# Optimization experiments

Hardware: AMD Instinct MI355X
Metric: run time of the kernel (lower is better)

The kernel has to match this reference:

```python
import jax, jax.numpy as jnp
import numpy as np

N_NODES = 100000
N_EDGES = 320000
EF_DIM = 128
HID = 128          # hidden_dim == time_dim
D_IN = EF_DIM + HID  # predictor input dim
Q = 4096


def setup_inputs() -> dict:
    key = jax.random.key(0)
    ks = jax.random.split(key, 16)
    src = jax.random.randint(ks[0], (N_EDGES,), 0, N_NODES, dtype=jnp.int32)
    dst = jax.random.randint(ks[1], (N_EDGES,), 0, N_NODES, dtype=jnp.int32)
    ef = jax.random.normal(ks[2], (N_EDGES, EF_DIM), dtype=jnp.float32)
    bt = jax.random.uniform(ks[3], (N_EDGES,), dtype=jnp.float32)
    node_ts = jax.random.uniform(ks[4], (N_NODES,), dtype=jnp.float32)
    s_idx = jax.random.randint(ks[5], (Q,), 0, N_NODES, dtype=jnp.int32)
    p_idx = jax.random.randint(ks[6], (Q,), 0, N_NODES, dtype=jnp.int32)
    n_idx = jax.random.randint(ks[7], (Q,), 0, N_NODES, dtype=jnp.int32)
    # TimeEncode weights: w = 1/10**linspace(0,9,HID), bias = 0
    time_w = jnp.asarray(1.0 / 10 ** np.linspace(0, 9, HID), dtype=jnp.float32)
    time_b = jnp.zeros((HID,), dtype=jnp.float32)
    sc1 = 1.0 / np.sqrt(D_IN)
    sc2 = 1.0 / np.sqrt(HID)
    W_src = jax.random.normal(ks[8], (D_IN, HID), dtype=jnp.float32) * sc1
    b_src = jnp.zeros((HID,), dtype=jnp.float32)
    W_dst = jax.random.normal(ks[9], (D_IN, HID), dtype=jnp.float32) * sc1
    b_dst = jnp.zeros((HID,), dtype=jnp.float32)
    W_out = jax.random.normal(ks[10], (HID, 1), dtype=jnp.float32) * sc2
    b_out = jnp.zeros((1,), dtype=jnp.float32)
    return {
        "src": src, "dst": dst, "ef": ef, "bt": bt, "node_ts": node_ts,
        "s_idx": s_idx, "p_idx": p_idx, "n_idx": n_idx,
        "time_w": time_w, "time_b": time_b,
        "W_src": W_src, "b_src": b_src,
        "W_dst": W_dst, "b_dst": b_dst,
        "W_out": W_out, "b_out": b_out,
    }


def reference(src, dst, ef, bt, node_ts, s_idx, p_idx, n_idx,
              time_w, time_b, W_src, b_src, W_dst, b_dst, W_out, b_out):
    n_nodes = node_ts.shape[0]
    # TemporalEdgePreprocess: time_diff = edge_ts - src_node_ts; cos(w*t + b)
    time_diff = bt - node_ts[src]                              # [E]
    tenc = jnp.cos(time_diff[:, None] * time_w[None, :] + time_b[None, :])  # [E, HID]
    efeat = jnp.concatenate([ef, tenc], axis=1)                # [E, D_IN]
    # update_all(copy_e, sum): segment-sum edge features into destination nodes
    h = jax.ops.segment_sum(efeat, dst, num_segments=n_nodes)  # [N, D_IN]
    s_emb = h[s_idx]                                           # [Q, D_IN]
    p_emb = h[p_idx]
    n_emb = h[n_idx]
    # EdgePredictor (neg_samples=1, so tile is identity)
    h_src = s_emb @ W_src + b_src
    h_pos = p_emb @ W_dst + b_dst
    h_neg = n_emb @ W_dst + b_dst
    pos_logit = jax.nn.relu(h_src + h_pos) @ W_out + b_out     # [Q, 1]
    neg_logit = jax.nn.relu(h_src + h_neg) @ W_out + b_out     # [Q, 1]
    return pos_logit, neg_logit
```

## Files before the change

kernel.cpp:

```cpp
#include <hip/hip_runtime.h>

#define N_NODES 100000
#define N_EDGES 320000
#define Q 4096
#define HID 128
#define DIN 256
#define EMB_LD 260
#define NSLOT (3 * Q)
#define CAP 64
#define QPB 8
#define KT 32

__global__ __launch_bounds__(256) void k_init(int4* __restrict__ slot4) {
    int i = blockIdx.x * 256 + threadIdx.x;
    if (i < N_NODES / 4) slot4[i] = make_int4(-1, -1, -1, -1);
}

__global__ __launch_bounds__(256) void k_claim(const int* __restrict__ s_idx,
                                               const int* __restrict__ p_idx,
                                               const int* __restrict__ n_idx,
                                               int* __restrict__ slot,
                                               int* __restrict__ cnt) {
    int i = blockIdx.x * 256 + threadIdx.x;
    cnt[i] = 0;
    int t = i >> 12;
    int q = i & (Q - 1);
    int node = (t == 0 ? s_idx : (t == 1 ? p_idx : n_idx))[q];
    atomicCAS(&slot[node], -1, i);
}

__global__ __launch_bounds__(256) void k_build(
    const int* __restrict__ src, const int* __restrict__ dst,
    const float* __restrict__ bt, const float* __restrict__ node_ts,
    const int* __restrict__ slot, int* __restrict__ cnt,
    int2* __restrict__ edata) {
    int e = blockIdx.x * 256 + threadIdx.x;
    if (e >= N_EDGES) return;
    int sl = slot[dst[e]];
    if (sl < 0) return;
    float td = bt[e] - node_ts[src[e]];
    int pos = atomicAdd(&cnt[sl], 1);
    if (pos < CAP) edata[sl * CAP + pos] = make_int2(e, __float_as_int(td));
}

__global__ __launch_bounds__(256) void k_fused(
    const int* __restrict__ s_idx, const int* __restrict__ p_idx,
    const int* __restrict__ n_idx, const int* __restrict__ slot,
    const int* __restrict__ cnt, const int2* __restrict__ edata,
    const float* __restrict__ ef,
    const float* __restrict__ time_w, const float* __restrict__ time_b,
    const float* __restrict__ W_src, const float* __restrict__ b_src,
    const float* __restrict__ W_dst, const float* __restrict__ b_dst,
    const float* __restrict__ W_out, const float* __restrict__ b_out,
    float* __restrict__ out) {
    __shared__ float emb[QPB * 3][EMB_LD];
    __shared__ float wstage[2][KT][HID];
    __shared__ float pP[QPB][4], pN[QPB][4];
    const int tid   = threadIdx.x;
    const int qbase = blockIdx.x * QPB;
    const int w     = tid >> 6;
    const int lane  = tid & 63;

    {
        const int j = lane >> 4;
        const int g = lane & 15;
        const float4 tw0 = *reinterpret_cast<const float4*>(time_w + 8 * g);
        const float4 tw1 = *reinterpret_cast<const float4*>(time_w + 8 * g + 4);
        const float4 tb0 = *reinterpret_cast<const float4*>(time_b + 8 * g);
        const float4 tb1 = *reinterpret_cast<const float4*>(time_b + 8 * g + 4);
        for (int row = w; row < QPB * 3; row += 4) {
            int t = row >> 3, q = row & 7;
            const int* ia = (t == 0) ? s_idx : (t == 1) ? p_idx : n_idx;
            int sl = slot[ia[qbase + q]];
            int n = cnt[sl]; if (n > CAP) n = CAP;
            float4 accA = {0.f, 0.f, 0.f, 0.f}, accB = {0.f, 0.f, 0.f, 0.f};
            float4 tcA  = {0.f, 0.f, 0.f, 0.f}, tcB  = {0.f, 0.f, 0.f, 0.f};
            for (int jb = j; jb < n; jb += 4) {
                int2 ed = edata[(size_t)sl * CAP + jb];
                const float* rp = ef + (size_t)ed.x * 128;
                float4 vA = *reinterpret_cast<const float4*>(rp + 4 * g);
                float4 vB = *reinterpret_cast<const float4*>(rp + 64 + 4 * g);
                float td = __int_as_float(ed.y);
                accA.x += vA.x; accA.y += vA.y; accA.z += vA.z; accA.w += vA.w;
                accB.x += vB.x; accB.y += vB.y; accB.z += vB.z; accB.w += vB.w;
                tcA.x += __cosf(td * tw0.x + tb0.x);
                tcA.y += __cosf(td * tw0.y + tb0.y);
                tcA.z += __cosf(td * tw0.z + tb0.z);
                tcA.w += __cosf(td * tw0.w + tb0.w);
                tcB.x += __cosf(td * tw1.x + tb1.x);
                tcB.y += __cosf(td * tw1.y + tb1.y);
                tcB.z += __cosf(td * tw1.z + tb1.z);
                tcB.w += __cosf(td * tw1.w + tb1.w);
            }
#define RED2(v) { v += __shfl_xor(v, 16); v += __shfl_xor(v, 32); }
            RED2(accA.x) RED2(accA.y) RED2(accA.z) RED2(accA.w)
            RED2(accB.x) RED2(accB.y) RED2(accB.z) RED2(accB.w)
            RED2(tcA.x)  RED2(tcA.y)  RED2(tcA.z)  RED2(tcA.w)
            RED2(tcB.x)  RED2(tcB.y)  RED2(tcB.z)  RED2(tcB.w)
#undef RED2
            if (j == 0) {
                *reinterpret_cast<float4*>(&emb[row][4 * g])       = accA;
                *reinterpret_cast<float4*>(&emb[row][64 + 4 * g])  = accB;
                *reinterpret_cast<float4*>(&emb[row][128 + 8 * g]) = tcA;
                *reinterpret_cast<float4*>(&emb[row][132 + 8 * g]) = tcB;
            }
        }
    }

    {
        const int q       = lane >> 3;
        const int g2      = lane & 7;
        const int colbase = 32 * w + 4 * g2;

        float4 bs = *reinterpret_cast<const float4*>(b_src + colbase);
        float4 bd = *reinterpret_cast<const float4*>(b_dst + colbase);
        float aS[4] = {bs.x, bs.y, bs.z, bs.w};
        float aP[4] = {bd.x, bd.y, bd.z, bd.w};
        float aN[4] = {bd.x, bd.y, bd.z, bd.w};

        const float* e_s = emb[q];
        const float* e_p = emb[QPB + q];
        const float* e_n = emb[2 * QPB + q];

        for (int kt = 0; kt < DIN; kt += KT) {
            __syncthreads();
            for (int r = tid; r < 2 * KT * HID / 4; r += 256) {
                int mat = r >> 10;
                int rem = r & 1023;
                int k   = rem >> 5;
                int c4  = rem & 31;
                const float* Wp = mat ? W_dst : W_src;
                float4 v = *reinterpret_cast<const float4*>(
                    Wp + (size_t)(kt + k) * HID + c4 * 4);
                *reinterpret_cast<float4*>(&wstage[mat][k][c4 * 4]) = v;
            }
            __syncthreads();
            for (int kk = 0; kk < KT; kk += 4) {
                float4 sv = *reinterpret_cast<const float4*>(e_s + kt + kk);
                float4 pv = *reinterpret_cast<const float4*>(e_p + kt + kk);
                float4 nv = *reinterpret_cast<const float4*>(e_n + kt + kk);
                #pragma unroll
                for (int k4 = 0; k4 < 4; ++k4) {
                    float4 ws = *reinterpret_cast<const float4*>(&wstage[0][kk + k4][colbase]);
                    float4 wd = *reinterpret_cast<const float4*>(&wstage[1][kk + k4][colbase]);
                    float s1 = (&sv.x)[k4], p1 = (&pv.x)[k4], n1 = (&nv.x)[k4];
                    #pragma unroll
                    for (int c = 0; c < 4; ++c) {
                        float wsc = (&ws.x)[c], wdc = (&wd.x)[c];
                        aS[c] += s1 * wsc;
                        aP[c] += p1 * wdc;
                        aN[c] += n1 * wdc;
                    }
                }
            }
        }

        float4 wo = *reinterpret_cast<const float4*>(W_out + colbase);
        float rP = 0.f, rN = 0.f;
        #pragma unroll
        for (int c = 0; c < 4; ++c) {
            float woc = (&wo.x)[c];
            rP += fmaxf(aS[c] + aP[c], 0.f) * woc;
            rN += fmaxf(aS[c] + aN[c], 0.f) * woc;
        }
        rP += __shfl_xor(rP, 1); rP += __shfl_xor(rP, 2); rP += __shfl_xor(rP, 4);
        rN += __shfl_xor(rN, 1); rN += __shfl_xor(rN, 2); rN += __shfl_xor(rN, 4);
        if (g2 == 0) { pP[q][w] = rP; pN[q][w] = rN; }
    }
    __syncthreads();

    if (tid < QPB) {
        float bo = b_out[0];
        out[qbase + tid]     = pP[tid][0] + pP[tid][1] + pP[tid][2] + pP[tid][3] + bo;
        out[Q + qbase + tid] = pN[tid][0] + pN[tid][1] + pN[tid][2] + pN[tid][3] + bo;
    }
}


extern "C" void kernel_launch(void* const* d_in, const int* in_sizes, int n_in,
                              void* d_out, int out_size, void* d_ws, size_t ws_size,
                              hipStream_t stream) {
    const int*   src     = (const int*)d_in[0];
    const int*   dst     = (const int*)d_in[1];
    const float* ef      = (const float*)d_in[2];
    const float* bt      = (const float*)d_in[3];
    const float* node_ts = (const float*)d_in[4];
    const int*   s_idx   = (const int*)d_in[5];
    const int*   p_idx   = (const int*)d_in[6];
    const int*   n_idx   = (const int*)d_in[7];
    const float* time_w  = (const float*)d_in[8];
    const float* time_b  = (const float*)d_in[9];
    const float* W_src   = (const float*)d_in[10];
    const float* b_src   = (const float*)d_in[11];
    const float* W_dst   = (const float*)d_in[12];
    const float* b_dst   = (const float*)d_in[13];
    const float* W_out   = (const float*)d_in[14];
    const float* b_out   = (const float*)d_in[15];
    float*       out     = (float*)d_out;

    char* ws = (char*)d_ws;
    int*   slot  = (int*)ws;
    int*   cnt   = (int*)(ws + 512 * 1024);
    int2*  edata = (int2*)(ws + 1024 * 1024);

    k_init<<<(N_NODES / 4 + 255) / 256, 256, 0, stream>>>((int4*)slot);
    k_claim<<<NSLOT / 256, 256, 0, stream>>>(s_idx, p_idx, n_idx, slot, cnt);
    k_build<<<(N_EDGES + 255) / 256, 256, 0, stream>>>(src, dst, bt, node_ts,
                                                       slot, cnt, edata);
    k_fused<<<Q / QPB, 256, 0, stream>>>(s_idx, p_idx, n_idx, slot, cnt,
                                         edata, ef, time_w, time_b,
                                         W_src, b_src, W_dst, b_dst,
                                         W_out, b_out, out);
}
```

Before: 50.53 us.

## Remap predictor GEMM threads to split-K halves with two queries per thread

```diff
diff --git a/kernel.cpp b/kernel.cpp
--- a/kernel.cpp
+++ b/kernel.cpp
@@ -55,7 +55,6 @@
     float* __restrict__ out) {
     __shared__ float emb[QPB * 3][EMB_LD];
     __shared__ float wstage[2][KT][HID];
-    __shared__ float pP[QPB][4], pN[QPB][4];
     const int tid   = threadIdx.x;
     const int qbase = blockIdx.x * QPB;
     const int w     = tid >> 6;
@@ -107,72 +106,114 @@
         }
     }
 
+    const int half    = tid >> 7;
+    const int hid     = tid & 127;
+    const int qp      = hid >> 5;
+    const int g2      = hid & 31;
+    const int colbase = g2 << 2;
+
+    float aS0[4], aS1[4], aP0[4], aP1[4], aN0[4], aN1[4];
     {
-        const int q       = lane >> 3;
-        const int g2      = lane & 7;
-        const int colbase = 32 * w + 4 * g2;
-
         float4 bs = *reinterpret_cast<const float4*>(b_src + colbase);
         float4 bd = *reinterpret_cast<const float4*>(b_dst + colbase);
-        float aS[4] = {bs.x, bs.y, bs.z, bs.w};
-        float aP[4] = {bd.x, bd.y, bd.z, bd.w};
-        float aN[4] = {bd.x, bd.y, bd.z, bd.w};
-
-        const float* e_s = emb[q];
-        const float* e_p = emb[QPB + q];
-        const float* e_n = emb[2 * QPB + q];
-
-        for (int kt = 0; kt < DIN; kt += KT) {
-            __syncthreads();
-            for (int r = tid; r < 2 * KT * HID / 4; r += 256) {
-                int mat = r >> 10;
-                int rem = r & 1023;
-                int k   = rem >> 5;
-                int c4  = rem & 31;
-                const float* Wp = mat ? W_dst : W_src;
-                float4 v = *reinterpret_cast<const float4*>(
-                    Wp + (size_t)(kt + k) * HID + c4 * 4);
-                *reinterpret_cast<float4*>(&wstage[mat][k][c4 * 4]) = v;
-            }
-            __syncthreads();
-            for (int kk = 0; kk < KT; kk += 4) {
-                float4 sv = *reinterpret_cast<const float4*>(e_s + kt + kk);
-                float4 pv = *reinterpret_cast<const float4*>(e_p + kt + kk);
-                float4 nv = *reinterpret_cast<const float4*>(e_n + kt + kk);
+        #pragma unroll
+        for (int c = 0; c < 4; ++c) {
+            float bsc = half ? 0.f : (&bs.x)[c];
+            float bdc = half ? 0.f : (&bd.x)[c];
+            aS0[c] = bsc; aS1[c] = bsc;
+            aP0[c] = bdc; aP1[c] = bdc;
+            aN0[c] = bdc; aN1[c] = bdc;
+        }
+    }
+
+    const float* e_s0 = emb[qp];
+    const float* e_s1 = emb[qp + 4];
+    const float* e_p0 = emb[QPB + qp];
+    const float* e_p1 = emb[QPB + qp + 4];
+    const float* e_n0 = emb[2 * QPB + qp];
+    const float* e_n1 = emb[2 * QPB + qp + 4];
+
+    for (int kt = 0; kt < DIN; kt += KT) {
+        __syncthreads();
+        for (int r = tid; r < 2 * KT * HID / 4; r += 256) {
+            int mat = r >> 10;
+            int rem = r & 1023;
+            int k   = rem >> 5;
+            int c4  = rem & 31;
+            const float* Wp = mat ? W_dst : W_src;
+            float4 v = *reinterpret_cast<const float4*>(
+                Wp + (size_t)(kt + k) * HID + c4 * 4);
+            *reinterpret_cast<float4*>(&wstage[mat][k][c4 * 4]) = v;
+        }
+        __syncthreads();
+        const int lk0 = half * (KT / 2);
+        const int kb  = kt + lk0;
+        for (int kk = 0; kk < KT / 2; kk += 4) {
+            float4 s0 = *reinterpret_cast<const float4*>(e_s0 + kb + kk);
+            float4 s1 = *reinterpret_cast<const float4*>(e_s1 + kb + kk);
+            float4 p0 = *reinterpret_cast<const float4*>(e_p0 + kb + kk);
+            float4 p1 = *reinterpret_cast<const float4*>(e_p1 + kb + kk);
+            float4 n0 = *reinterpret_cast<const float4*>(e_n0 + kb + kk);
+            float4 n1 = *reinterpret_cast<const float4*>(e_n1 + kb + kk);
+            #pragma unroll
+            for (int k4 = 0; k4 < 4; ++k4) {
+                float4 ws = *reinterpret_cast<const float4*>(&wstage[0][lk0 + kk + k4][colbase]);
+                float4 wd = *reinterpret_cast<const float4*>(&wstage[1][lk0 + kk + k4][colbase]);
+                float sv0 = (&s0.x)[k4], sv1 = (&s1.x)[k4];
+                float pv0 = (&p0.x)[k4], pv1 = (&p1.x)[k4];
+                float nv0 = (&n0.x)[k4], nv1 = (&n1.x)[k4];
                 #pragma unroll
-                for (int k4 = 0; k4 < 4; ++k4) {
-                    float4 ws = *reinterpret_cast<const float4*>(&wstage[0][kk + k4][colbase]);
-                    float4 wd = *reinterpret_cast<const float4*>(&wstage[1][kk + k4][colbase]);
-                    float s1 = (&sv.x)[k4], p1 = (&pv.x)[k4], n1 = (&nv.x)[k4];
-                    #pragma unroll
-                    for (int c = 0; c < 4; ++c) {
-                        float wsc = (&ws.x)[c], wdc = (&wd.x)[c];
-                        aS[c] += s1 * wsc;
-                        aP[c] += p1 * wdc;
-                        aN[c] += n1 * wdc;
-                    }
+                for (int c = 0; c < 4; ++c) {
+                    float wsc = (&ws.x)[c], wdc = (&wd.x)[c];
+                    aS0[c] += sv0 * wsc;  aS1[c] += sv1 * wsc;
+                    aP0[c] += pv0 * wdc;  aP1[c] += pv1 * wdc;
+                    aN0[c] += nv0 * wdc;  aN1[c] += nv1 * wdc;
                 }
             }
         }
-
+    }
+
+    float (*part)[24] = reinterpret_cast<float(*)[24]>(&emb[0][0]);
+    __syncthreads();
+    if (half) {
+        float* p = part[hid];
+        #pragma unroll
+        for (int c = 0; c < 4; ++c) {
+            p[c]      = aS0[c]; p[4 + c]  = aS1[c];
+            p[8 + c]  = aP0[c]; p[12 + c] = aP1[c];
+            p[16 + c] = aN0[c]; p[20 + c] = aN1[c];
+        }
+    }
+    __syncthreads();
+    if (!half) {
+        const float* p = part[hid];
         float4 wo = *reinterpret_cast<const float4*>(W_out + colbase);
-        float rP = 0.f, rN = 0.f;
+        float rP0 = 0.f, rN0 = 0.f, rP1 = 0.f, rN1 = 0.f;
         #pragma unroll
         for (int c = 0; c < 4; ++c) {
+            float sc0 = aS0[c] + p[c],      sc1 = aS1[c] + p[4 + c];
+            float pc0 = aP0[c] + p[8 + c],  pc1 = aP1[c] + p[12 + c];
+            float nc0 = aN0[c] + p[16 + c], nc1 = aN1[c] + p[20 + c];
             float woc = (&wo.x)[c];
-            rP += fmaxf(aS[c] + aP[c], 0.f) * woc;
-            rN += fmaxf(aS[c] + aN[c], 0.f) * woc;
-        }
-        rP += __shfl_xor(rP, 1); rP += __shfl_xor(rP, 2); rP += __shfl_xor(rP, 4);
-        rN += __shfl_xor(rN, 1); rN += __shfl_xor(rN, 2); rN += __shfl_xor(rN, 4);
-        if (g2 == 0) { pP[q][w] = rP; pN[q][w] = rN; }
-    }
-    __syncthreads();
-
-    if (tid < QPB) {
-        float bo = b_out[0];
-        out[qbase + tid]     = pP[tid][0] + pP[tid][1] + pP[tid][2] + pP[tid][3] + bo;
-        out[Q + qbase + tid] = pN[tid][0] + pN[tid][1] + pN[tid][2] + pN[tid][3] + bo;
+            rP0 += fmaxf(sc0 + pc0, 0.f) * woc;
+            rN0 += fmaxf(sc0 + nc0, 0.f) * woc;
+            rP1 += fmaxf(sc1 + pc1, 0.f) * woc;
+            rN1 += fmaxf(sc1 + nc1, 0.f) * woc;
+        }
+        #pragma unroll
+        for (int off = 1; off < 32; off <<= 1) {
+            rP0 += __shfl_xor(rP0, off);
+            rN0 += __shfl_xor(rN0, off);
+            rP1 += __shfl_xor(rP1, off);
+            rN1 += __shfl_xor(rN1, off);
+        }
+        if (g2 == 0) {
+            float bo = b_out[0];
+            out[qbase + qp]         = rP0 + bo;
+            out[Q + qbase + qp]     = rN0 + bo;
+            out[qbase + qp + 4]     = rP1 + bo;
+            out[Q + qbase + qp + 4] = rN1 + bo;
+        }
     }
 }
 
```

Measured after the change: 49.21 us (median of 3 runs). -2.6%, faster.

## Restructure predictor GEMM as split-K register tiles with swizzled weight staging

Applied to the files above, without the earlier changes.

```diff
diff --git a/kernel.cpp b/kernel.cpp
--- a/kernel.cpp
+++ b/kernel.cpp
@@ -55,10 +55,9 @@
     float* __restrict__ out) {
     __shared__ float emb[QPB * 3][EMB_LD];
     __shared__ float wstage[2][KT][HID];
-    __shared__ float pP[QPB][4], pN[QPB][4];
     const int tid   = threadIdx.x;
     const int qbase = blockIdx.x * QPB;
-    const int w     = tid >> 6;
+    const int wv    = tid >> 6;
     const int lane  = tid & 63;
 
     {
@@ -68,7 +67,7 @@
         const float4 tw1 = *reinterpret_cast<const float4*>(time_w + 8 * g + 4);
         const float4 tb0 = *reinterpret_cast<const float4*>(time_b + 8 * g);
         const float4 tb1 = *reinterpret_cast<const float4*>(time_b + 8 * g + 4);
-        for (int row = w; row < QPB * 3; row += 4) {
+        for (int row = wv; row < QPB * 3; row += 4) {
             int t = row >> 3, q = row & 7;
             const int* ia = (t == 0) ? s_idx : (t == 1) ? p_idx : n_idx;
             int sl = slot[ia[qbase + q]];
@@ -107,72 +106,137 @@
         }
     }
 
-    {
-        const int q       = lane >> 3;
-        const int g2      = lane & 7;
-        const int colbase = 32 * w + 4 * g2;
-
-        float4 bs = *reinterpret_cast<const float4*>(b_src + colbase);
-        float4 bd = *reinterpret_cast<const float4*>(b_dst + colbase);
-        float aS[4] = {bs.x, bs.y, bs.z, bs.w};
-        float aP[4] = {bd.x, bd.y, bd.z, bd.w};
-        float aN[4] = {bd.x, bd.y, bd.z, bd.w};
-
-        const float* e_s = emb[q];
-        const float* e_p = emb[QPB + q];
-        const float* e_n = emb[2 * QPB + q];
-
-        for (int kt = 0; kt < DIN; kt += KT) {
-            __syncthreads();
-            for (int r = tid; r < 2 * KT * HID / 4; r += 256) {
-                int mat = r >> 10;
-                int rem = r & 1023;
-                int k   = rem >> 5;
-                int c4  = rem & 31;
-                const float* Wp = mat ? W_dst : W_src;
-                float4 v = *reinterpret_cast<const float4*>(
-                    Wp + (size_t)(kt + k) * HID + c4 * 4);
-                *reinterpret_cast<float4*>(&wstage[mat][k][c4 * 4]) = v;
-            }
-            __syncthreads();
-            for (int kk = 0; kk < KT; kk += 4) {
-                float4 sv = *reinterpret_cast<const float4*>(e_s + kt + kk);
-                float4 pv = *reinterpret_cast<const float4*>(e_p + kt + kk);
-                float4 nv = *reinterpret_cast<const float4*>(e_n + kt + kk);
+    const int g3      = tid & 15;
+    const int ksl     = (tid >> 4) & 3;
+    const int qg      = wv & 1;
+    const int ksh     = wv >> 1;
+    const int ks      = ksh * 4 + ksl;
+    const int colbase = g3 * 8;
+
+    float aS[4][8], aP[4][8], aN[4][8];
+    #pragma unroll
+    for (int qi = 0; qi < 4; ++qi)
+        #pragma unroll
+        for (int c = 0; c < 8; ++c) { aS[qi][c] = 0.f; aP[qi][c] = 0.f; aN[qi][c] = 0.f; }
+    if (ks == 0) {
+        #pragma unroll
+        for (int c = 0; c < 8; ++c) {
+            float bs = b_src[colbase + c], bd = b_dst[colbase + c];
+            #pragma unroll
+            for (int qi = 0; qi < 4; ++qi) { aS[qi][c] = bs; aP[qi][c] = bd; aN[qi][c] = bd; }
+        }
+    }
+
+    const int kb = ks * 4;
+    const int u0 = (g3 * 2) ^ ksl;
+    const int u1 = (g3 * 2 + 1) ^ ksl;
+
+    for (int kt = 0; kt < DIN; kt += KT) {
+        __syncthreads();
+        for (int r = tid; r < 2 * KT * HID / 4; r += 256) {
+            int mat = r >> 10;
+            int rem = r & 1023;
+            int k   = rem >> 5;
+            int c4  = rem & 31;
+            const float* Wp = mat ? W_dst : W_src;
+            float4 v = *reinterpret_cast<const float4*>(
+                Wp + (size_t)(kt + k) * HID + c4 * 4);
+            int c4s = c4 ^ ((k >> 2) & 3);
+            *reinterpret_cast<float4*>(&wstage[mat][k][c4s * 4]) = v;
+        }
+        __syncthreads();
+
+        float4 es[4], ep[4], en[4];
+        #pragma unroll
+        for (int qi = 0; qi < 4; ++qi) {
+            int qrow = qg * 4 + qi;
+            es[qi] = *reinterpret_cast<const float4*>(&emb[qrow][kt + kb]);
+            ep[qi] = *reinterpret_cast<const float4*>(&emb[QPB + qrow][kt + kb]);
+            en[qi] = *reinterpret_cast<const float4*>(&emb[2 * QPB + qrow][kt + kb]);
+        }
+        #pragma unroll
+        for (int kk = 0; kk < 4; ++kk) {
+            int k = kb + kk;
+            float4 ws0 = *reinterpret_cast<const float4*>(&wstage[0][k][u0 * 4]);
+            float4 ws1 = *reinterpret_cast<const float4*>(&wstage[0][k][u1 * 4]);
+            float4 wd0 = *reinterpret_cast<const float4*>(&wstage[1][k][u0 * 4]);
+            float4 wd1 = *reinterpret_cast<const float4*>(&wstage[1][k][u1 * 4]);
+            #pragma unroll
+            for (int qi = 0; qi < 4; ++qi) {
+                float sv = (&es[qi].x)[kk];
+                float pv = (&ep[qi].x)[kk];
+                float nv = (&en[qi].x)[kk];
                 #pragma unroll
-                for (int k4 = 0; k4 < 4; ++k4) {
-                    float4 ws = *reinterpret_cast<const float4*>(&wstage[0][kk + k4][colbase]);
-                    float4 wd = *reinterpret_cast<const float4*>(&wstage[1][kk + k4][colbase]);
-                    float s1 = (&sv.x)[k4], p1 = (&pv.x)[k4], n1 = (&nv.x)[k4];
-                    #pragma unroll
-                    for (int c = 0; c < 4; ++c) {
-                        float wsc = (&ws.x)[c], wdc = (&wd.x)[c];
-                        aS[c] += s1 * wsc;
-                        aP[c] += p1 * wdc;
-                        aN[c] += n1 * wdc;
-                    }
+                for (int c = 0; c < 4; ++c) {
+                    aS[qi][c]     += sv * (&ws0.x)[c];
+                    aS[qi][4 + c] += sv * (&ws1.x)[c];
+                    aP[qi][c]     += pv * (&wd0.x)[c];
+                    aP[qi][4 + c] += pv * (&wd1.x)[c];
+                    aN[qi][c]     += nv * (&wd0.x)[c];
+                    aN[qi][4 + c] += nv * (&wd1.x)[c];
                 }
             }
         }
-
-        float4 wo = *reinterpret_cast<const float4*>(W_out + colbase);
-        float rP = 0.f, rN = 0.f;
-        #pragma unroll
-        for (int c = 0; c < 4; ++c) {
-            float woc = (&wo.x)[c];
-            rP += fmaxf(aS[c] + aP[c], 0.f) * woc;
-            rN += fmaxf(aS[c] + aN[c], 0.f) * woc;
-        }
-        rP += __shfl_xor(rP, 1); rP += __shfl_xor(rP, 2); rP += __shfl_xor(rP, 4);
-        rN += __shfl_xor(rN, 1); rN += __shfl_xor(rN, 2); rN += __shfl_xor(rN, 4);
-        if (g2 == 0) { pP[q][w] = rP; pN[q][w] = rN; }
-    }
+    }
+
+    #pragma unroll
+    for (int qi = 0; qi < 4; ++qi)
+        #pragma unroll
+        for (int c = 0; c < 8; ++c) {
+            float s = aS[qi][c]; s += __shfl_xor(s, 16); s += __shfl_xor(s, 32); aS[qi][c] = s;
+            float p = aP[qi][c]; p += __shfl_xor(p, 16); p += __shfl_xor(p, 32); aP[qi][c] = p;
+            float n = aN[qi][c]; n += __shfl_xor(n, 16); n += __shfl_xor(n, 32); aN[qi][c] = n;
+        }
+
+    float* ov = &emb[0][0];
     __syncthreads();
-
-    if (tid < QPB) {
-        float bo = b_out[0];
-        out[qbase + tid]     = pP[tid][0] + pP[tid][1] + pP[tid][2] + pP[tid][3] + bo;
-        out[Q + qbase + tid] = pN[tid][0] + pN[tid][1] + pN[tid][2] + pN[tid][3] + bo;
+    if (ksh == 1 && ksl == 0) {
+        float* p = ov + (qg * 16 + g3) * 97;
+        #pragma unroll
+        for (int qi = 0; qi < 4; ++qi)
+            #pragma unroll
+            for (int c = 0; c < 8; ++c) {
+                p[qi * 24 + c]      = aS[qi][c];
+                p[qi * 24 + 8 + c]  = aP[qi][c];
+                p[qi * 24 + 16 + c] = aN[qi][c];
+            }
+    }
+    __syncthreads();
+    if (ksh == 0 && ksl == 0) {
+        const float* p = ov + (qg * 16 + g3) * 97;
+        float4 wo0 = *reinterpret_cast<const float4*>(W_out + colbase);
+        float4 wo1 = *reinterpret_cast<const float4*>(W_out + colbase + 4);
+        float rP[4], rN[4];
+        #pragma unroll
+        for (int qi = 0; qi < 4; ++qi) {
+            float sp = 0.f, sn = 0.f;
+            #pragma unroll
+            for (int c = 0; c < 8; ++c) {
+                float sc = aS[qi][c] + p[qi * 24 + c];
+                float pc = aP[qi][c] + p[qi * 24 + 8 + c];
+                float nc = aN[qi][c] + p[qi * 24 + 16 + c];
+                float woc = (c < 4) ? (&wo0.x)[c] : (&wo1.x)[c - 4];
+                sp += fmaxf(sc + pc, 0.f) * woc;
+                sn += fmaxf(sc + nc, 0.f) * woc;
+            }
+            rP[qi] = sp; rN[qi] = sn;
+        }
+        #pragma unroll
+        for (int off = 1; off < 16; off <<= 1) {
+            #pragma unroll
+            for (int qi = 0; qi < 4; ++qi) {
+                rP[qi] += __shfl_xor(rP[qi], off);
+                rN[qi] += __shfl_xor(rN[qi], off);
+            }
+        }
+        if (g3 == 0) {
+            float bo = b_out[0];
+            #pragma unroll
+            for (int qi = 0; qi < 4; ++qi) {
+                out[qbase + qg * 4 + qi]     = rP[qi] + bo;
+                out[Q + qbase + qg * 4 + qi] = rN[qi] + bo;
+            }
+        }
     }
 }
 
```

New measurement: 81.09 us. +60.5%, slower.
